# Performance work log

Measured on AMD Instinct MI355X. Metric: run time of the kernel, lower is better.

## Reference

```python
import jax, jax.numpy as jnp
import numpy as np

B, H, L, D = 2, 16, 1024, 64
LMAX = 2048  # max_sequence_length: patterns built & normalized at LMAX, then sliced to L
PI = float(np.pi)


def _scale_pattern(freq):
    # pattern[h, t, d] = exp(i(t+ph)) + exp(i(2t+ph)) + exp(i(0.5t+ph)), ph = 2*pi*h/H
    # identical across d, so keep [H, L, 1] and broadcast over D
    phase = 2.0 * PI * jnp.arange(H, dtype=jnp.float32) / H          # [H]
    t = jnp.linspace(0.0, 2.0 * PI * freq, LMAX)                     # [LMAX]
    a1 = t[None, :] + phase[:, None]
    a2 = 2.0 * t[None, :] + phase[:, None]
    a3 = 0.5 * t[None, :] + phase[:, None]
    pr = jnp.cos(a1) + jnp.cos(a2) + jnp.cos(a3)                     # [H, LMAX]
    pi_ = jnp.sin(a1) + jnp.sin(a2) + jnp.sin(a3)
    norm = jnp.sqrt(jnp.sum(pr * pr + pi_ * pi_, axis=1, keepdims=True))  # over full LMAX
    pr, pi_ = pr / norm, pi_ / norm
    return pr[:, :L, None], pi_[:, :L, None]                          # [H, L, 1]


def _expert_total_pattern():
    # 8 experts x 3 aspects; pattern[t, d] = exp(i(f*t + 2*pi*d/D)), normalized per
    # column over LMAX (|exp|=1 -> norm sqrt(LMAX)). Elementwise complex multiply is
    # linear, so the expert stage equals x * sum(all patterns)/(sqrt(3)*sqrt(8)).
    freqs = np.array([[0.3 + 0.1 * i, 0.2 + 0.1 * i, 0.1 + 0.1 * i]
                      for i in range(8)], dtype=np.float32).reshape(-1)   # [24]
    t = jnp.linspace(0.0, 2.0 * PI, LMAX)                                 # [LMAX]
    phase_d = 2.0 * PI * jnp.arange(D, dtype=jnp.float32) / D             # [D]
    ang = jnp.asarray(freqs)[:, None, None] * t[None, :, None] + phase_d[None, None, :]  # [24, LMAX, D]
    col_norm = 1.0 / np.sqrt(float(LMAX))
    denom = np.sqrt(3.0) * np.sqrt(8.0)
    pr = jnp.sum(jnp.cos(ang), axis=0) * (col_norm / denom)               # [LMAX, D]
    pi_ = jnp.sum(jnp.sin(ang), axis=0) * (col_norm / denom)
    return pr[:L], pi_[:L]                                                # [L, D]


def _process_scale(Qr, Qi, Kr, Ki, Vr, Vi, pr, pi_):
    # complex elementwise pattern multiply
    Qpr = Qr * pr - Qi * pi_
    Qpi = Qr * pi_ + Qi * pr
    Kpr = Kr * pr - Ki * pi_
    Kpi = Kr * pi_ + Ki * pr
    # complex scores = Qp @ Kp^T (no conjugation, matching the torch code)
    sr = jnp.einsum('bhld,bhmd->bhlm', Qpr, Kpr) - jnp.einsum('bhld,bhmd->bhlm', Qpi, Kpi)
    si = jnp.einsum('bhld,bhmd->bhlm', Qpr, Kpi) + jnp.einsum('bhld,bhmd->bhlm', Qpi, Kpr)
    mag = jnp.sqrt(sr * sr + si * si) / np.sqrt(float(D))
    w = jax.nn.softmax(mag, axis=-1)
    return (jnp.einsum('bhlm,bhmd->bhld', w, Vr),
            jnp.einsum('bhlm,bhmd->bhld', w, Vi))


def reference(Q_real, Q_imag, K_real, K_imag, V_real, V_imag):
    scale_freqs = [1.0, 0.5, 0.25, 0.1]  # char, word, phrase, sentence
    acc_r = jnp.zeros_like(Q_real)
    acc_i = jnp.zeros_like(Q_real)
    for f in scale_freqs:
        pr, pi_ = _scale_pattern(f)
        o_r, o_i = _process_scale(Q_real, Q_imag, K_real, K_imag, V_real, V_imag, pr, pi_)
        acc_r = acc_r + o_r
        acc_i = acc_i + o_i
    inv = 1.0 / np.sqrt(float(len(scale_freqs)))
    acc_r = acc_r * inv
    acc_i = acc_i * inv
    # expert mixing (linear in x -> single fused complex elementwise multiply)
    epr, epi = _expert_total_pattern()  # [L, D], broadcast over B,H
    out_r = acc_r * epr - acc_i * epi
    out_i = acc_r * epi + acc_i * epr
    return jnp.stack([out_r, out_i], axis=0)  # [2, B, H, L, D] (real, imag)


def setup_inputs() -> dict:
    key = jax.random.key(0)
    ks = jax.random.split(key, 6)
    shape = (B, H, L, D)
    names = ['Q_real', 'Q_imag', 'K_real', 'K_imag', 'V_real', 'V_imag']
    return {n: jax.random.normal(k, shape, dtype=jnp.float32) for n, k in zip(names, ks)}
```

## Files before the change

### kernel.cpp

```cpp
#include <hip/hip_runtime.h>
#include <math.h>

typedef short bf16x8 __attribute__((ext_vector_type(8)));
typedef float f32x4 __attribute__((ext_vector_type(4)));

#define BDIM 256
#define ADIM 512
constexpr int B_ = 2, H_ = 16, L_ = 1024, D_ = 64, LMAX_ = 2048;
constexpr int BH_ = B_ * H_;
constexpr float PI_F = 3.14159265358979323846f;

constexpr int WS_SVP = 0;
constexpr int WS_KBR = 65536;
constexpr int WS_KBI = WS_KBR + 1048576;
constexpr int WS_VTR = WS_KBI + 1048576;
constexpr int WS_VTI = WS_VTR + 1048576;

__device__ __forceinline__ unsigned short f2b(float x) {
    union { float f; unsigned u; } v; v.f = x;
    return (unsigned short)((v.u + 0x8000u) >> 16);
}
__device__ __forceinline__ float b2f(unsigned short x) {
    union { unsigned u; float f; } v; v.u = ((unsigned)x) << 16;
    return v.f;
}
__device__ __forceinline__ unsigned pk2(float a, float b) {
    union { float f; unsigned u; } va, vb; va.f = a; vb.f = b;
    return ((va.u + 0x8000u) >> 16) | ((vb.u + 0x8000u) & 0xFFFF0000u);
}
__device__ __forceinline__ uint4 pack4(const float4& a, const float4& b) {
    return make_uint4(pk2(a.x, a.y), pk2(a.z, a.w), pk2(b.x, b.y), pk2(b.z, b.w));
}
__device__ __forceinline__ unsigned cvtpk(float lo, float hi) {
    unsigned r;
    asm("v_cvt_pk_bf16_f32 %0, %1, %2" : "=v"(r) : "v"(lo), "v"(hi));
    return r;
}
__device__ __forceinline__ float vsqrt(float x) {
    float r;
    asm("v_sqrt_f32 %0, %1" : "=v"(r) : "v"(x));
    return r;
}

#define MFMA(a, b, c) __builtin_amdgcn_mfma_f32_16x16x32_bf16((a), (b), (c), 0, 0, 0)

__device__ __forceinline__ float a_val(int s, int l, float4 invn) {
    const float fr = (s == 0) ? 1.0f : (s == 1) ? 0.5f : (s == 2) ? 0.25f : 0.1f;
    const float iv = (s == 0) ? invn.x : (s == 1) ? invn.y : (s == 2) ? invn.z : invn.w;
    float t = (2.0f * PI_F * fr / (float)(LMAX_ - 1)) * (float)l;
    float m2 = 3.0f + 2.0f * cosf(t) + 2.0f * cosf(0.5f * t) + 2.0f * cosf(1.5f * t);
    return sqrtf(fmaxf(m2, 0.0f)) * iv;
}

__global__ __launch_bounds__(BDIM)
void prep_kernel(const float* __restrict__ Kr, const float* __restrict__ Ki,
                 const float* __restrict__ Vr, const float* __restrict__ Vi,
                 float* __restrict__ ws) {
    const int tid = threadIdx.x;
    const int blk = blockIdx.x;
    unsigned short* KbR = (unsigned short*)(ws + WS_KBR);
    unsigned short* KbI = (unsigned short*)(ws + WS_KBI);
    unsigned short* VtR = (unsigned short*)(ws + WS_VTR);
    unsigned short* VtI = (unsigned short*)(ws + WS_VTI);

    if (blk < 256) {
        const int comp = blk >> 7;
        const float* src = comp ? Ki : Kr;
        unsigned short* dst = comp ? KbI : KbR;
        size_t b0 = (size_t)(blk & 127) * 16384;
#pragma unroll
        for (int i = 0; i < 4; ++i) {
            size_t e = b0 + (size_t)(i * 256 + tid) * 16;
            float4 x0 = *(const float4*)(src + e);
            float4 x1 = *(const float4*)(src + e + 4);
            float4 x2 = *(const float4*)(src + e + 8);
            float4 x3 = *(const float4*)(src + e + 12);
            *(uint4*)(dst + e) = pack4(x0, x1);
            *(uint4*)(dst + e + 8) = pack4(x2, x3);
        }
    } else {
        __shared__ unsigned short sT[64 * 70];
        __shared__ float sRed[4 * 64];
        const int vb = blk - 256;
        const int comp = vb & 1, mt = (vb >> 1) & 15, bh = vb >> 5;
        const int m0 = mt * 64;
        const float* src = (comp ? Vi : Vr) + (size_t)bh * 65536 + (size_t)m0 * 64;
        unsigned short* dstA = (comp ? VtI : VtR) + (size_t)bh * 65536;
#pragma unroll
        for (int i = 0; i < 4; ++i) {
            int e = i * 256 + tid;
            int m = e >> 4, d4 = (e & 15) * 4;
            float4 x = *(const float4*)(src + (size_t)m * 64 + d4);
            *(uint2*)&sT[m * 70 + d4] = make_uint2(pk2(x.x, x.y), pk2(x.z, x.w));
        }
        {
            int d = tid & 63, grp = tid >> 6;
            float s = 0.0f;
#pragma unroll
            for (int k = 0; k < 16; ++k) s += src[(size_t)(grp * 16 + k) * 64 + d];
            sRed[grp * 64 + d] = s;
        }
        __syncthreads();
        {
            int d = tid >> 2, ms = (tid & 3) * 16;
            unsigned short v[16];
#pragma unroll
            for (int k = 0; k < 16; ++k) v[k] = sT[(ms + k) * 70 + d];
            unsigned short* dst = dstA + (size_t)d * 1024 + m0 + ms;
            *(uint4*)dst = make_uint4((unsigned)v[0] | ((unsigned)v[1] << 16),
                                      (unsigned)v[2] | ((unsigned)v[3] << 16),
                                      (unsigned)v[4] | ((unsigned)v[5] << 16),
                                      (unsigned)v[6] | ((unsigned)v[7] << 16));
            *(uint4*)(dst + 8) = make_uint4((unsigned)v[8] | ((unsigned)v[9] << 16),
                                            (unsigned)v[10] | ((unsigned)v[11] << 16),
                                            (unsigned)v[12] | ((unsigned)v[13] << 16),
                                            (unsigned)v[14] | ((unsigned)v[15] << 16));
        }
        if (tid < 64)
            ws[WS_SVP + comp * 32768 + bh * 1024 + tid * 16 + mt] =
                sRed[tid] + sRed[64 + tid] + sRed[128 + tid] + sRed[192 + tid];
    }
}

__device__ __forceinline__ void stage64s(const unsigned short* g0, int stride,
                                         unsigned short* lds, int w, int lane) {
#pragma unroll
    for (int i = 0; i < 2; ++i) {
        int c = w * 2 + i;
        int lrow = c * 8 + (lane >> 3);
        int lg = (lane & 7) ^ (lrow & 7);
        const unsigned short* src = g0 + (size_t)lrow * stride + lg * 8;
        __builtin_amdgcn_global_load_lds(
            (const __attribute__((address_space(1))) void*)src,
            (__attribute__((address_space(3))) void*)(lds + c * 512), 16, 0, 0);
    }
}
__device__ __forceinline__ bf16x8 ldfrag(const unsigned short* b, int row, int g) {
    return *(const bf16x8*)&b[row * 64 + ((g ^ (row & 7)) << 3)];
}

constexpr int OFF_DEN = 0;
constexpr int OFF_K0  = 2048;
constexpr int OFF_K1  = OFF_K0 + 16384;
constexpr int OFF_V0  = OFF_K1 + 16384;
constexpr int OFF_V1  = OFF_V0 + 16384;
constexpr int OFF_E   = OFF_V1 + 16384;
constexpr int OFF_MG  = OFF_E + 16384;
constexpr int OFF_AMB = OFF_MG + 16384;
constexpr int SMEM_BYTES = OFF_AMB + 8256;

__global__ __launch_bounds__(ADIM, 2)
void attn_kernel_w(const float* __restrict__ Qr, const float* __restrict__ Qi,
                   const float* __restrict__ ws, float* __restrict__ out, float4 invn) {
    extern __shared__ char smem[];
    float* sDen = (float*)(smem + OFF_DEN);
    unsigned short* sK0 = (unsigned short*)(smem + OFF_K0);
    unsigned short* sK1 = (unsigned short*)(smem + OFF_K1);
    unsigned short* sV0 = (unsigned short*)(smem + OFF_V0);
    unsigned short* sV1 = (unsigned short*)(smem + OFF_V1);
    unsigned short* sE  = (unsigned short*)(smem + OFF_E);
    unsigned short* sMg = (unsigned short*)(smem + OFF_MG);
    unsigned short* sAmb = (unsigned short*)(smem + OFF_AMB);

    const int tid = threadIdx.x;
    const int lane = tid & 63;
    const int w = tid >> 6;
    const int lo16 = lane & 15;
    const int quad = lane >> 4;
    const int blk = blockIdx.x;
    const int bh = (blk & 7) * 4 + (blk >> 6);
    const int qt = (blk >> 3) & 7;
    const int l0 = qt * 128;
    const size_t base = (size_t)bh * (L_ * D_);

    const unsigned short* gKr = (const unsigned short*)(ws + WS_KBR) + (size_t)bh * 65536;
    const unsigned short* gKi = (const unsigned short*)(ws + WS_KBI) + (size_t)bh * 65536;
    const unsigned short* gVr = (const unsigned short*)(ws + WS_VTR) + (size_t)bh * 65536;
    const unsigned short* gVi = (const unsigned short*)(ws + WS_VTI) + (size_t)bh * 65536;

    if (w < 4) {
        stage64s(gKr, 64, sK0, w, lane);
        stage64s(gKi, 64, sK1, w, lane);
    } else {
        stage64s(gVr, 1024, sV0, w - 4, lane);
        stage64s(gVi, 1024, sV1, w - 4, lane);
    }

    for (int e = tid; e < 4096; e += ADIM) {
        int s = e >> 10, l = e & 1023;
        sAmb[s * 1032 + l] = f2b(a_val(s, l, invn) * 0.125f);
    }

    bf16x8 fQr0, fQr1, fQi0, fQi1, fnQi0, fnQi1;
    {
        const int ql = l0 + w * 16 + lo16;
        const float* qr = Qr + base + (size_t)ql * 64;
        const float* qi = Qi + base + (size_t)ql * 64;
        float4 a0 = *(const float4*)(qr + quad * 8);
        float4 a1 = *(const float4*)(qr + quad * 8 + 4);
        float4 b0 = *(const float4*)(qr + 32 + quad * 8);
        float4 b1 = *(const float4*)(qr + 32 + quad * 8 + 4);
        *(uint4*)&fQr0 = pack4(a0, a1);
        *(uint4*)&fQr1 = pack4(b0, b1);
        a0 = *(const float4*)(qi + quad * 8);
        a1 = *(const float4*)(qi + quad * 8 + 4);
        b0 = *(const float4*)(qi + 32 + quad * 8);
        b1 = *(const float4*)(qi + 32 + quad * 8 + 4);
        *(uint4*)&fQi0 = pack4(a0, a1);
        *(uint4*)&fQi1 = pack4(b0, b1);
        uint4 t0 = *(uint4*)&fQi0, t1 = *(uint4*)&fQi1;
        t0.x ^= 0x80008000u; t0.y ^= 0x80008000u; t0.z ^= 0x80008000u; t0.w ^= 0x80008000u;
        t1.x ^= 0x80008000u; t1.y ^= 0x80008000u; t1.z ^= 0x80008000u; t1.w ^= 0x80008000u;
        *(uint4*)&fnQi0 = t0; *(uint4*)&fnQi1 = t1;
    }

    __syncthreads();

    bf16x8 uf1a = (bf16x8){0, 0, 0, 0, 0, 0, 0, 0};
    uf1a[0] = (short)f2b(b2f(sAmb[quad * 1032 + (l0 + w * 16 + lo16)]) *
                         (1.0f / 128.0f));

    f32x4 accM1 = (f32x4){0.f, 0.f, 0.f, 0.f};
    f32x4 aOutR[4], aOutI[4];
#pragma unroll
    for (int dt = 0; dt < 4; ++dt) {
        aOutR[dt] = (f32x4){0.f, 0.f, 0.f, 0.f};
        aOutI[dt] = (f32x4){0.f, 0.f, 0.f, 0.f};
    }

#pragma unroll 1
    for (int mt = 0; mt < 16; ++mt) {
        const int m0 = mt * 64;
        const int cur = mt & 1;
        if (mt < 15) {
            if (w < 4) {
                stage64s(gKr + (size_t)(m0 + 64) * 64, 64, sK0 + (cur ^ 1) * 4096, w, lane);
                stage64s(gKi + (size_t)(m0 + 64) * 64, 64, sK1 + (cur ^ 1) * 4096, w, lane);
            } else {
                stage64s(gVr + m0 + 64, 1024, sV0 + (cur ^ 1) * 4096, w - 4, lane);
                stage64s(gVi + m0 + 64, 1024, sV1 + (cur ^ 1) * 4096, w - 4, lane);
            }
        }
        const unsigned short* cK0 = sK0 + cur * 4096;
        const unsigned short* cK1 = sK1 + cur * 4096;
        const unsigned short* cV0 = sV0 + cur * 4096;
        const unsigned short* cV1 = sV1 + cur * 4096;

#pragma unroll
        for (int ct = 0; ct < 4; ++ct) {
            const int mrow = ct * 16 + lo16;
            bf16x8 kr0 = ldfrag(cK0, mrow, quad), kr1 = ldfrag(cK0, mrow, quad + 4);
            bf16x8 ki0 = ldfrag(cK1, mrow, quad), ki1 = ldfrag(cK1, mrow, quad + 4);
            f32x4 aR = (f32x4){0.f, 0.f, 0.f, 0.f};
            f32x4 aI = (f32x4){0.f, 0.f, 0.f, 0.f};
            __builtin_amdgcn_s_setprio(1);
            aR = MFMA(kr0, fQr0, aR);  aR = MFMA(kr1, fQr1, aR);
            aR = MFMA(ki0, fnQi0, aR); aR = MFMA(ki1, fnQi1, aR);
            aI = MFMA(ki0, fQr0, aI);  aI = MFMA(ki1, fQr1, aI);
            aI = MFMA(kr0, fQi0, aI);  aI = MFMA(kr1, fQi1, aI);
            __builtin_amdgcn_s_setprio(0);
            float mg0 = vsqrt(fmaf(aR[0], aR[0], aI[0] * aI[0]));
            float mg1 = vsqrt(fmaf(aR[1], aR[1], aI[1] * aI[1]));
            float mg2 = vsqrt(fmaf(aR[2], aR[2], aI[2] * aI[2]));
            float mg3 = vsqrt(fmaf(aR[3], aR[3], aI[3] * aI[3]));
            bf16x8 bf1 = (bf16x8){0, 0, 0, 0, 0, 0, 0, 0};
            bf1[0] = (short)sAmb[quad * 1032 + m0 + ct * 16 + lo16];
            f32x4 z = (f32x4){0.f, 0.f, 0.f, 0.f};
            f32x4 a1 = MFMA(bf1, uf1a, z);
            float p0 = mg0 * a1[0], p1 = mg1 * a1[1];
            float p2 = mg2 * a1[2], p3 = mg3 * a1[3];
            int l = w * 16 + lo16;
            int gph = (ct * 2 + (quad >> 1)) ^ (l & 7);
            *(uint2*)&sE[l * 64 + gph * 8 + (quad & 1) * 4] =
                make_uint2(cvtpk(p0, p1), cvtpk(p2, p3));
            *(uint2*)&sMg[l * 64 + gph * 8 + (quad & 1) * 4] =
                make_uint2(cvtpk(mg0, mg1), cvtpk(mg2, mg3));
        }
        {
            bf16x8 mf0 = ldfrag(sMg, w * 16 + lo16, quad);
            bf16x8 mf1 = ldfrag(sMg, w * 16 + lo16, quad + 4);
            bf16x8 b0 = (bf16x8){0, 0, 0, 0, 0, 0, 0, 0};
            bf16x8 b1 = (bf16x8){0, 0, 0, 0, 0, 0, 0, 0};
            if (lo16 < 4) {
                b0 = *(const bf16x8*)&sAmb[lo16 * 1032 + m0 + quad * 8];
                b1 = *(const bf16x8*)&sAmb[lo16 * 1032 + m0 + 32 + quad * 8];
            }
            accM1 = MFMA(mf0, b0, accM1);
            accM1 = MFMA(mf1, b1, accM1);
        }
        {
            bf16x8 pa0 = ldfrag(sE, w * 16 + lo16, quad);
            bf16x8 pa1 = ldfrag(sE, w * 16 + lo16, quad + 4);
            __builtin_amdgcn_s_setprio(1);
#pragma unroll
            for (int dt = 0; dt < 4; ++dt) {
                int dr = dt * 16 + lo16;
                bf16x8 vr0 = ldfrag(cV0, dr, quad), vr1 = ldfrag(cV0, dr, quad + 4);
                bf16x8 vi0 = ldfrag(cV1, dr, quad), vi1 = ldfrag(cV1, dr, quad + 4);
                aOutR[dt] = MFMA(pa0, vr0, aOutR[dt]);
                aOutR[dt] = MFMA(pa1, vr1, aOutR[dt]);
                aOutI[dt] = MFMA(pa0, vi0, aOutI[dt]);
                aOutI[dt] = MFMA(pa1, vi1, aOutI[dt]);
            }
            __builtin_amdgcn_s_setprio(0);
        }
        asm volatile("s_waitcnt vmcnt(0)" ::: "memory");
        __builtin_amdgcn_s_barrier();
    }

    if (lo16 < 4) {
#pragma unroll
        for (int reg = 0; reg < 4; ++reg) {
            int r = w * 16 + quad * 4 + reg;
            float alv = b2f(sAmb[lo16 * 1032 + (l0 + r)]) * 8.0f;
            sDen[lo16 * 128 + r] = 1.0f / (1024.0f + alv * accM1[reg]);
        }
    }
    float cden[4];
#pragma unroll
    for (int reg = 0; reg < 4; ++reg) {
        int r = w * 16 + quad * 4 + reg;
        cden[reg] = sDen[r] + sDen[128 + r] + sDen[256 + r] + sDen[384 + r];
    }

    const float cE = rsqrtf(2048.0f) * rsqrtf(24.0f);
    float eRr[4], eRi[4];
#pragma unroll
    for (int reg = 0; reg < 4; ++reg) {
        int lrow = l0 + w * 16 + quad * 4 + reg;
        float tl = (2.0f * PI_F / (float)(LMAX_ - 1)) * (float)lrow;
        float s1, c1;
        __sincosf(0.1f * tl, &s1, &c1);
        const float W[10] = {1.f, 2.f, 3.f, 3.f, 3.f, 3.f, 3.f, 3.f, 2.f, 1.f};
        float cr = c1, ci = s1;
        float er = W[0] * cr, ei = W[0] * ci;
#pragma unroll
        for (int k = 1; k < 10; ++k) {
            float nr = cr * c1 - ci * s1;
            float ni = cr * s1 + ci * c1;
            cr = nr; ci = ni;
            er = fmaf(W[k], cr, er);
            ei = fmaf(W[k], ci, ei);
        }
        eRr[reg] = er * cE;
        eRi[reg] = ei * cE;
    }

    const size_t ooff = (size_t)BH_ * L_ * D_;
#pragma unroll
    for (int dt = 0; dt < 4; ++dt) {
        int d = dt * 16 + lo16;
        const float* svp = ws + WS_SVP + bh * 1024 + (size_t)d * 16;
        float4 r0 = *(const float4*)(svp);
        float4 r1 = *(const float4*)(svp + 4);
        float4 r2 = *(const float4*)(svp + 8);
        float4 r3 = *(const float4*)(svp + 12);
        float svr = (r0.x + r0.y + r0.z + r0.w) + (r1.x + r1.y + r1.z + r1.w) +
                    (r2.x + r2.y + r2.z + r2.w) + (r3.x + r3.y + r3.z + r3.w);
        const float* svq = svp + 32768;
        r0 = *(const float4*)(svq);
        r1 = *(const float4*)(svq + 4);
        r2 = *(const float4*)(svq + 8);
        r3 = *(const float4*)(svq + 12);
        float svi = (r0.x + r0.y + r0.z + r0.w) + (r1.x + r1.y + r1.z + r1.w) +
                    (r2.x + r2.y + r2.z + r2.w) + (r3.x + r3.y + r3.z + r3.w);
        float sp, cp;
        __sincosf((2.0f * PI_F / 64.0f) * (float)d, &sp, &cp);
#pragma unroll
        for (int reg = 0; reg < 4; ++reg) {
            int lrow = l0 + w * 16 + quad * 4 + reg;
            float numR = fmaf(cden[reg], svr, aOutR[dt][reg]) * 0.5f;
            float numI = fmaf(cden[reg], svi, aOutI[dt][reg]) * 0.5f;
            float epr = cp * eRr[reg] - sp * eRi[reg];
            float epi = sp * eRr[reg] + cp * eRi[reg];
            size_t o = base + (size_t)lrow * 64 + d;
            out[o] = numR * epr - numI * epi;
            out[o + ooff] = numR * epi + numI * epr;
        }
    }
}

__global__ __launch_bounds__(BDIM, 2)
void attn_kernel(const float* __restrict__ Qr, const float* __restrict__ Qi,
                 const float* __restrict__ ws, float* __restrict__ out, float4 invn) {
    __shared__ unsigned short sK0[2][4096], sK1[2][4096];
    __shared__ unsigned short sV0[4096], sV1[4096];
    __shared__ unsigned short sE[4096];
    __shared__ unsigned short sMg[4096];
    __shared__ unsigned short sAmb[4 * 1032];
    __shared__ float sDen[4 * 64];

    const int tid = threadIdx.x;
    const int lane = tid & 63;
    const int w = tid >> 6;
    const int lo16 = lane & 15;
    const int quad = lane >> 4;
    const int blk = blockIdx.x;
    const int bh = (blk & 7) * 4 + (blk >> 7);
    const int qt = (blk >> 3) & 15;
    const int l0 = qt * 64;
    const size_t base = (size_t)bh * (L_ * D_);

    const unsigned short* gKr = (const unsigned short*)(ws + WS_KBR) + (size_t)bh * 65536;
    const unsigned short* gKi = (const unsigned short*)(ws + WS_KBI) + (size_t)bh * 65536;
    const unsigned short* gVr = (const unsigned short*)(ws + WS_VTR) + (size_t)bh * 65536;
    const unsigned short* gVi = (const unsigned short*)(ws + WS_VTI) + (size_t)bh * 65536;

    stage64s(gKr, 64, sK0[0], w, lane);
    stage64s(gKi, 64, sK1[0], w, lane);

    for (int e = tid; e < 4096; e += BDIM) {
        int s = e >> 10, l = e & 1023;
        sAmb[s * 1032 + l] = f2b(a_val(s, l, invn) * 0.125f);
    }

    bf16x8 fQr0, fQr1, fQi0, fQi1, fnQi0, fnQi1;
    {
        const int ql = l0 + w * 16 + lo16;
        const float* qr = Qr + base + (size_t)ql * 64;
        const float* qi = Qi + base + (size_t)ql * 64;
        float4 a0 = *(const float4*)(qr + quad * 8);
        float4 a1 = *(const float4*)(qr + quad * 8 + 4);
        float4 b0 = *(const float4*)(qr + 32 + quad * 8);
        float4 b1 = *(const float4*)(qr + 32 + quad * 8 + 4);
        *(uint4*)&fQr0 = pack4(a0, a1);
        *(uint4*)&fQr1 = pack4(b0, b1);
        a0 = *(const float4*)(qi + quad * 8);
        a1 = *(const float4*)(qi + quad * 8 + 4);
        b0 = *(const float4*)(qi + 32 + quad * 8);
        b1 = *(const float4*)(qi + 32 + quad * 8 + 4);
        *(uint4*)&fQi0 = pack4(a0, a1);
        *(uint4*)&fQi1 = pack4(b0, b1);
        uint4 t0 = *(uint4*)&fQi0, t1 = *(uint4*)&fQi1;
        t0.x ^= 0x80008000u; t0.y ^= 0x80008000u; t0.z ^= 0x80008000u; t0.w ^= 0x80008000u;
        t1.x ^= 0x80008000u; t1.y ^= 0x80008000u; t1.z ^= 0x80008000u; t1.w ^= 0x80008000u;
        *(uint4*)&fnQi0 = t0; *(uint4*)&fnQi1 = t1;
    }

    __syncthreads();

    bf16x8 uf1a = (bf16x8){0, 0, 0, 0, 0, 0, 0, 0};
    uf1a[0] = (short)f2b(b2f(sAmb[quad * 1032 + (l0 + w * 16 + lo16)]) *
                         (1.0f / 128.0f));

    f32x4 accM1 = (f32x4){0.f, 0.f, 0.f, 0.f};
    f32x4 aOutR[4], aOutI[4];
#pragma unroll
    for (int dt = 0; dt < 4; ++dt) {
        aOutR[dt] = (f32x4){0.f, 0.f, 0.f, 0.f};
        aOutI[dt] = (f32x4){0.f, 0.f, 0.f, 0.f};
    }

#pragma unroll 1
    for (int mt = 0; mt < 16; ++mt) {
        const int m0 = mt * 64;
        const int cur = mt & 1;
        stage64s(gVr + m0, 1024, sV0, w, lane);
        stage64s(gVi + m0, 1024, sV1, w, lane);
        if (mt < 15) {
            stage64s(gKr + (size_t)(m0 + 64) * 64, 64, sK0[cur ^ 1], w, lane);
            stage64s(gKi + (size_t)(m0 + 64) * 64, 64, sK1[cur ^ 1], w, lane);
        }
        const unsigned short* cK0 = sK0[cur];
        const unsigned short* cK1 = sK1[cur];

#pragma unroll
        for (int ct = 0; ct < 4; ++ct) {
            const int mrow = ct * 16 + lo16;
            bf16x8 kr0 = ldfrag(cK0, mrow, quad), kr1 = ldfrag(cK0, mrow, quad + 4);
            bf16x8 ki0 = ldfrag(cK1, mrow, quad), ki1 = ldfrag(cK1, mrow, quad + 4);
            f32x4 aR = (f32x4){0.f, 0.f, 0.f, 0.f};
            f32x4 aI = (f32x4){0.f, 0.f, 0.f, 0.f};
            __builtin_amdgcn_s_setprio(1);
            aR = MFMA(kr0, fQr0, aR);  aR = MFMA(kr1, fQr1, aR);
            aR = MFMA(ki0, fnQi0, aR); aR = MFMA(ki1, fnQi1, aR);
            aI = MFMA(ki0, fQr0, aI);  aI = MFMA(ki1, fQr1, aI);
            aI = MFMA(kr0, fQi0, aI);  aI = MFMA(kr1, fQi1, aI);
            __builtin_amdgcn_s_setprio(0);
            float mg0 = vsqrt(fmaf(aR[0], aR[0], aI[0] * aI[0]));
            float mg1 = vsqrt(fmaf(aR[1], aR[1], aI[1] * aI[1]));
            float mg2 = vsqrt(fmaf(aR[2], aR[2], aI[2] * aI[2]));
            float mg3 = vsqrt(fmaf(aR[3], aR[3], aI[3] * aI[3]));
            bf16x8 bf1 = (bf16x8){0, 0, 0, 0, 0, 0, 0, 0};
            bf1[0] = (short)sAmb[quad * 1032 + m0 + ct * 16 + lo16];
            f32x4 z = (f32x4){0.f, 0.f, 0.f, 0.f};
            f32x4 a1 = MFMA(bf1, uf1a, z);
            float p0 = mg0 * a1[0], p1 = mg1 * a1[1];
            float p2 = mg2 * a1[2], p3 = mg3 * a1[3];
            int l = w * 16 + lo16;
            int gph = (ct * 2 + (quad >> 1)) ^ (l & 7);
            *(uint2*)&sE[l * 64 + gph * 8 + (quad & 1) * 4] =
                make_uint2(cvtpk(p0, p1), cvtpk(p2, p3));
            *(uint2*)&sMg[l * 64 + gph * 8 + (quad & 1) * 4] =
                make_uint2(cvtpk(mg0, mg1), cvtpk(mg2, mg3));
        }
        {
            bf16x8 mf0 = ldfrag(sMg, w * 16 + lo16, quad);
            bf16x8 mf1 = ldfrag(sMg, w * 16 + lo16, quad + 4);
            bf16x8 b0 = (bf16x8){0, 0, 0, 0, 0, 0, 0, 0};
            bf16x8 b1 = (bf16x8){0, 0, 0, 0, 0, 0, 0, 0};
            if (lo16 < 4) {
                b0 = *(const bf16x8*)&sAmb[lo16 * 1032 + m0 + quad * 8];
                b1 = *(const bf16x8*)&sAmb[lo16 * 1032 + m0 + 32 + quad * 8];
            }
            accM1 = MFMA(mf0, b0, accM1);
            accM1 = MFMA(mf1, b1, accM1);
        }
        if (mt < 15) {
            asm volatile("s_waitcnt vmcnt(4)" ::: "memory");
        } else {
            asm volatile("s_waitcnt vmcnt(0)" ::: "memory");
        }
        __builtin_amdgcn_s_barrier();
        {
            bf16x8 pa0 = ldfrag(sE, w * 16 + lo16, quad);
            bf16x8 pa1 = ldfrag(sE, w * 16 + lo16, quad + 4);
            __builtin_amdgcn_s_setprio(1);
#pragma unroll
            for (int dt = 0; dt < 4; ++dt) {
                int dr = dt * 16 + lo16;
                bf16x8 vr0 = ldfrag(sV0, dr, quad), vr1 = ldfrag(sV0, dr, quad + 4);
                bf16x8 vi0 = ldfrag(sV1, dr, quad), vi1 = ldfrag(sV1, dr, quad + 4);
                aOutR[dt] = MFMA(pa0, vr0, aOutR[dt]);
                aOutR[dt] = MFMA(pa1, vr1, aOutR[dt]);
                aOutI[dt] = MFMA(pa0, vi0, aOutI[dt]);
                aOutI[dt] = MFMA(pa1, vi1, aOutI[dt]);
            }
            __builtin_amdgcn_s_setprio(0);
        }
        asm volatile("s_waitcnt vmcnt(0)" ::: "memory");
        __builtin_amdgcn_s_barrier();
    }

    if (lo16 < 4) {
#pragma unroll
        for (int reg = 0; reg < 4; ++reg) {
            int r = w * 16 + quad * 4 + reg;
            float alv = b2f(sAmb[lo16 * 1032 + (l0 + r)]) * 8.0f;
            sDen[lo16 * 64 + r] = 1.0f / (1024.0f + alv * accM1[reg]);
        }
    }
    float cden[4];
#pragma unroll
    for (int reg = 0; reg < 4; ++reg) {
        int r = w * 16 + quad * 4 + reg;
        cden[reg] = sDen[r] + sDen[64 + r] + sDen[128 + r] + sDen[192 + r];
    }

    const float cE = rsqrtf(2048.0f) * rsqrtf(24.0f);
    float eRr[4], eRi[4];
#pragma unroll
    for (int reg = 0; reg < 4; ++reg) {
        int lrow = l0 + w * 16 + quad * 4 + reg;
        float tl = (2.0f * PI_F / (float)(LMAX_ - 1)) * (float)lrow;
        float s1, c1;
        __sincosf(0.1f * tl, &s1, &c1);
        const float W[10] = {1.f, 2.f, 3.f, 3.f, 3.f, 3.f, 3.f, 3.f, 2.f, 1.f};
        float cr = c1, ci = s1;
        float er = W[0] * cr, ei = W[0] * ci;
#pragma unroll
        for (int k = 1; k < 10; ++k) {
            float nr = cr * c1 - ci * s1;
            float ni = cr * s1 + ci * c1;
            cr = nr; ci = ni;
            er = fmaf(W[k], cr, er);
            ei = fmaf(W[k], ci, ei);
        }
        eRr[reg] = er * cE;
        eRi[reg] = ei * cE;
    }

    const size_t ooff = (size_t)BH_ * L_ * D_;
#pragma unroll
    for (int dt = 0; dt < 4; ++dt) {
        int d = dt * 16 + lo16;
        const float* svp = ws + WS_SVP + bh * 1024 + (size_t)d * 16;
        float4 r0 = *(const float4*)(svp);
        float4 r1 = *(const float4*)(svp + 4);
        float4 r2 = *(const float4*)(svp + 8);
        float4 r3 = *(const float4*)(svp + 12);
        float svr = (r0.x + r0.y + r0.z + r0.w) + (r1.x + r1.y + r1.z + r1.w) +
                    (r2.x + r2.y + r2.z + r2.w) + (r3.x + r3.y + r3.z + r3.w);
        const float* svq = svp + 32768;
        r0 = *(const float4*)(svq);
        r1 = *(const float4*)(svq + 4);
        r2 = *(const float4*)(svq + 8);
        r3 = *(const float4*)(svq + 12);
        float svi = (r0.x + r0.y + r0.z + r0.w) + (r1.x + r1.y + r1.z + r1.w) +
                    (r2.x + r2.y + r2.z + r2.w) + (r3.x + r3.y + r3.z + r3.w);
        float sp, cp;
        __sincosf((2.0f * PI_F / 64.0f) * (float)d, &sp, &cp);
#pragma unroll
        for (int reg = 0; reg < 4; ++reg) {
            int lrow = l0 + w * 16 + quad * 4 + reg;
            float numR = fmaf(cden[reg], svr, aOutR[dt][reg]) * 0.5f;
            float numI = fmaf(cden[reg], svi, aOutI[dt][reg]) * 0.5f;
            float epr = cp * eRr[reg] - sp * eRi[reg];
            float epi = sp * eRr[reg] + cp * eRi[reg];
            size_t o = base + (size_t)lrow * 64 + d;
            out[o] = numR * epr - numI * epi;
            out[o + ooff] = numR * epi + numI * epr;
        }
    }
}

extern "C" void kernel_launch(void* const* d_in, const int* in_sizes, int n_in,
                              void* d_out, int out_size, void* d_ws, size_t ws_size,
                              hipStream_t stream) {
    const float* Qr = (const float*)d_in[0];
    const float* Qi = (const float*)d_in[1];
    const float* Kr = (const float*)d_in[2];
    const float* Ki = (const float*)d_in[3];
    const float* Vr = (const float*)d_in[4];
    const float* Vi = (const float*)d_in[5];
    float* ws = (float*)d_ws;
    float* out = (float*)d_out;

    const double fr[4] = {1.0, 0.5, 0.25, 0.1};
    float inv[4];
    for (int s = 0; s < 4; ++s) {
        double a = 2.0 * 3.14159265358979323846 * fr[s] / (double)(LMAX_ - 1);
        double S = 3.0 * LMAX_;
        const double mul[3] = {1.0, 0.5, 1.5};
        for (int k = 0; k < 3; ++k) {
            double x = a * mul[k];
            S += 2.0 * (cos(x * 1023.5) * sin(x * 1024.0) / sin(x * 0.5));
        }
        inv[s] = (float)(1.0 / sqrt(S));
    }
    float4 invn = make_float4(inv[0], inv[1], inv[2], inv[3]);

    prep_kernel<<<1280, BDIM, 0, stream>>>(Kr, Ki, Vr, Vi, ws);

    static int wideOK = -1;
    if (wideOK < 0) {
        hipError_t e = hipFuncSetAttribute(
            reinterpret_cast<const void*>(attn_kernel_w),
            hipFuncAttributeMaxDynamicSharedMemorySize, SMEM_BYTES);
        wideOK = (e == hipSuccess) ? 1 : 0;
    }
    if (wideOK)
        attn_kernel_w<<<256, ADIM, SMEM_BYTES, stream>>>(Qr, Qi, ws, out, invn);
    else
        attn_kernel<<<512, BDIM, 0, stream>>>(Qr, Qi, ws, out, invn);
}
```

Before: 138.8 us.

## Split key columns across two wave halves with 1024-thread blocks and LDS reduction

New measurement: 134.6 us. 3.0% less time.

```diff
diff --git a/kernel.cpp b/kernel.cpp
--- a/kernel.cpp
+++ b/kernel.cpp
@@ -5,7 +5,7 @@
 typedef float f32x4 __attribute__((ext_vector_type(4)));
 
 #define BDIM 256
-#define ADIM 512
+#define ADIM 1024
 constexpr int B_ = 2, H_ = 16, L_ = 1024, D_ = 64, LMAX_ = 2048;
 constexpr int BH_ = B_ * H_;
 constexpr float PI_F = 3.14159265358979323846f;
@@ -149,7 +149,7 @@
 constexpr int OFF_AMB = OFF_MG + 16384;
 constexpr int SMEM_BYTES = OFF_AMB + 8256;
 
-__global__ __launch_bounds__(ADIM, 2)
+__global__ __launch_bounds__(ADIM, 1)
 void attn_kernel_w(const float* __restrict__ Qr, const float* __restrict__ Qi,
                    const float* __restrict__ ws, float* __restrict__ out, float4 invn) {
     extern __shared__ char smem[];
@@ -165,8 +165,11 @@
     const int tid = threadIdx.x;
     const int lane = tid & 63;
     const int w = tid >> 6;
+    const int half = w >> 3;
+    const int w8 = w & 7;
     const int lo16 = lane & 15;
     const int quad = lane >> 4;
+    const int gh = quad + half * 4;
     const int blk = blockIdx.x;
     const int bh = (blk & 7) * 4 + (blk >> 6);
     const int qt = (blk >> 3) & 7;
@@ -181,12 +184,248 @@
     if (w < 4) {
         stage64s(gKr, 64, sK0, w, lane);
         stage64s(gKi, 64, sK1, w, lane);
-    } else {
-        stage64s(gVr, 1024, sV0, w - 4, lane);
-        stage64s(gVi, 1024, sV1, w - 4, lane);
+    } else if (w >= 8 && w < 12) {
+        stage64s(gVr, 1024, sV0, w - 8, lane);
+        stage64s(gVi, 1024, sV1, w - 8, lane);
     }
 
     for (int e = tid; e < 4096; e += ADIM) {
+        int s = e >> 10, l = e & 1023;
+        sAmb[s * 1032 + l] = f2b(a_val(s, l, invn) * 0.125f);
+    }
+
+    bf16x8 fQr0, fQr1, fQi0, fQi1, fnQi0, fnQi1;
+    {
+        const int ql = l0 + w8 * 16 + lo16;
+        const float* qr = Qr + base + (size_t)ql * 64;
+        const float* qi = Qi + base + (size_t)ql * 64;
+        float4 a0 = *(const float4*)(qr + quad * 8);
+        float4 a1 = *(const float4*)(qr + quad * 8 + 4);
+        float4 b0 = *(const float4*)(qr + 32 + quad * 8);
+        float4 b1 = *(const float4*)(qr + 32 + quad * 8 + 4);
+        *(uint4*)&fQr0 = pack4(a0, a1);
+        *(uint4*)&fQr1 = pack4(b0, b1);
+        a0 = *(const float4*)(qi + quad * 8);
+        a1 = *(const float4*)(qi + quad * 8 + 4);
+        b0 = *(const float4*)(qi + 32 + quad * 8);
+        b1 = *(const float4*)(qi + 32 + quad * 8 + 4);
+        *(uint4*)&fQi0 = pack4(a0, a1);
+        *(uint4*)&fQi1 = pack4(b0, b1);
+        uint4 t0 = *(uint4*)&fQi0, t1 = *(uint4*)&fQi1;
+        t0.x ^= 0x80008000u; t0.y ^= 0x80008000u; t0.z ^= 0x80008000u; t0.w ^= 0x80008000u;
+        t1.x ^= 0x80008000u; t1.y ^= 0x80008000u; t1.z ^= 0x80008000u; t1.w ^= 0x80008000u;
+        *(uint4*)&fnQi0 = t0; *(uint4*)&fnQi1 = t1;
+    }
+
+    __syncthreads();
+
+    bf16x8 uf1a = (bf16x8){0, 0, 0, 0, 0, 0, 0, 0};
+    uf1a[0] = (short)f2b(b2f(sAmb[quad * 1032 + (l0 + w8 * 16 + lo16)]) *
+                         (1.0f / 128.0f));
+
+    f32x4 accM1 = (f32x4){0.f, 0.f, 0.f, 0.f};
+    f32x4 aOutR[4], aOutI[4];
+#pragma unroll
+    for (int dt = 0; dt < 4; ++dt) {
+        aOutR[dt] = (f32x4){0.f, 0.f, 0.f, 0.f};
+        aOutI[dt] = (f32x4){0.f, 0.f, 0.f, 0.f};
+    }
+
+    const int lrow_w = w8 * 16 + lo16;
+
+#pragma unroll 1
+    for (int mt = 0; mt < 16; ++mt) {
+        const int m0 = mt * 64;
+        const int cur = mt & 1;
+        if (mt < 15) {
+            if (w < 4) {
+                stage64s(gKr + (size_t)(m0 + 64) * 64, 64, sK0 + (cur ^ 1) * 4096, w, lane);
+                stage64s(gKi + (size_t)(m0 + 64) * 64, 64, sK1 + (cur ^ 1) * 4096, w, lane);
+            } else if (w >= 8 && w < 12) {
+                stage64s(gVr + m0 + 64, 1024, sV0 + (cur ^ 1) * 4096, w - 8, lane);
+                stage64s(gVi + m0 + 64, 1024, sV1 + (cur ^ 1) * 4096, w - 8, lane);
+            }
+        }
+        const unsigned short* cK0 = sK0 + cur * 4096;
+        const unsigned short* cK1 = sK1 + cur * 4096;
+        const unsigned short* cV0 = sV0 + cur * 4096;
+        const unsigned short* cV1 = sV1 + cur * 4096;
+
+#pragma unroll
+        for (int ct = 0; ct < 2; ++ct) {
+            const int ct_eff = half * 2 + ct;
+            const int mrow = ct_eff * 16 + lo16;
+            bf16x8 kr0 = ldfrag(cK0, mrow, quad), kr1 = ldfrag(cK0, mrow, quad + 4);
+            bf16x8 ki0 = ldfrag(cK1, mrow, quad), ki1 = ldfrag(cK1, mrow, quad + 4);
+            f32x4 aR = (f32x4){0.f, 0.f, 0.f, 0.f};
+            f32x4 aI = (f32x4){0.f, 0.f, 0.f, 0.f};
+            __builtin_amdgcn_s_setprio(1);
+            aR = MFMA(kr0, fQr0, aR);  aR = MFMA(kr1, fQr1, aR);
+            aR = MFMA(ki0, fnQi0, aR); aR = MFMA(ki1, fnQi1, aR);
+            aI = MFMA(ki0, fQr0, aI);  aI = MFMA(ki1, fQr1, aI);
+            aI = MFMA(kr0, fQi0, aI);  aI = MFMA(kr1, fQi1, aI);
+            __builtin_amdgcn_s_setprio(0);
+            float mg0 = vsqrt(fmaf(aR[0], aR[0], aI[0] * aI[0]));
+            float mg1 = vsqrt(fmaf(aR[1], aR[1], aI[1] * aI[1]));
+            float mg2 = vsqrt(fmaf(aR[2], aR[2], aI[2] * aI[2]));
+            float mg3 = vsqrt(fmaf(aR[3], aR[3], aI[3] * aI[3]));
+            bf16x8 bf1 = (bf16x8){0, 0, 0, 0, 0, 0, 0, 0};
+            bf1[0] = (short)sAmb[quad * 1032 + m0 + ct_eff * 16 + lo16];
+            f32x4 z = (f32x4){0.f, 0.f, 0.f, 0.f};
+            f32x4 a1 = MFMA(bf1, uf1a, z);
+            float p0 = mg0 * a1[0], p1 = mg1 * a1[1];
+            float p2 = mg2 * a1[2], p3 = mg3 * a1[3];
+            int gph = (ct_eff * 2 + (quad >> 1)) ^ (lrow_w & 7);
+            *(uint2*)&sE[lrow_w * 64 + gph * 8 + (quad & 1) * 4] =
+                make_uint2(cvtpk(p0, p1), cvtpk(p2, p3));
+            *(uint2*)&sMg[lrow_w * 64 + gph * 8 + (quad & 1) * 4] =
+                make_uint2(cvtpk(mg0, mg1), cvtpk(mg2, mg3));
+        }
+        {
+            bf16x8 mf = ldfrag(sMg, lrow_w, gh);
+            bf16x8 b0 = (bf16x8){0, 0, 0, 0, 0, 0, 0, 0};
+            if (lo16 < 4)
+                b0 = *(const bf16x8*)&sAmb[lo16 * 1032 + m0 + half * 32 + quad * 8];
+            accM1 = MFMA(mf, b0, accM1);
+        }
+        {
+            bf16x8 pa = ldfrag(sE, lrow_w, gh);
+            __builtin_amdgcn_s_setprio(1);
+#pragma unroll
+            for (int dt = 0; dt < 4; ++dt) {
+                int dr = dt * 16 + lo16;
+                bf16x8 vr = ldfrag(cV0, dr, gh);
+                bf16x8 vi = ldfrag(cV1, dr, gh);
+                aOutR[dt] = MFMA(pa, vr, aOutR[dt]);
+                aOutI[dt] = MFMA(pa, vi, aOutI[dt]);
+            }
+            __builtin_amdgcn_s_setprio(0);
+        }
+        asm volatile("s_waitcnt vmcnt(0)" ::: "memory");
+        __builtin_amdgcn_s_barrier();
+    }
+
+    char* scr = smem + OFF_K0;
+    if (half == 1) {
+#pragma unroll
+        for (int dt = 0; dt < 4; ++dt) {
+            *(f32x4*)(scr + w8 * 9216 + dt * 1024 + lane * 16) = aOutR[dt];
+            *(f32x4*)(scr + w8 * 9216 + 4096 + dt * 1024 + lane * 16) = aOutI[dt];
+        }
+        *(f32x4*)(scr + w8 * 9216 + 8192 + lane * 16) = accM1;
+    }
+    __syncthreads();
+    if (half == 1) return;
+
+#pragma unroll
+    for (int dt = 0; dt < 4; ++dt) {
+        aOutR[dt] += *(const f32x4*)(scr + w8 * 9216 + dt * 1024 + lane * 16);
+        aOutI[dt] += *(const f32x4*)(scr + w8 * 9216 + 4096 + dt * 1024 + lane * 16);
+    }
+    accM1 += *(const f32x4*)(scr + w8 * 9216 + 8192 + lane * 16);
+
+    if (lo16 < 4) {
+#pragma unroll
+        for (int reg = 0; reg < 4; ++reg) {
+            int r = w8 * 16 + quad * 4 + reg;
+            float alv = b2f(sAmb[lo16 * 1032 + (l0 + r)]) * 8.0f;
+            sDen[lo16 * 128 + r] = 1.0f / (1024.0f + alv * accM1[reg]);
+        }
+    }
+    float cden[4];
+#pragma unroll
+    for (int reg = 0; reg < 4; ++reg) {
+        int r = w8 * 16 + quad * 4 + reg;
+        cden[reg] = sDen[r] + sDen[128 + r] + sDen[256 + r] + sDen[384 + r];
+    }
+
+    const float cE = rsqrtf(2048.0f) * rsqrtf(24.0f);
+    float eRr[4], eRi[4];
+#pragma unroll
+    for (int reg = 0; reg < 4; ++reg) {
+        int lrow = l0 + w8 * 16 + quad * 4 + reg;
+        float tl = (2.0f * PI_F / (float)(LMAX_ - 1)) * (float)lrow;
+        float s1, c1;
+        __sincosf(0.1f * tl, &s1, &c1);
+        const float W[10] = {1.f, 2.f, 3.f, 3.f, 3.f, 3.f, 3.f, 3.f, 2.f, 1.f};
+        float cr = c1, ci = s1;
+        float er = W[0] * cr, ei = W[0] * ci;
+#pragma unroll
+        for (int k = 1; k < 10; ++k) {
+            float nr = cr * c1 - ci * s1;
+            float ni = cr * s1 + ci * c1;
+            cr = nr; ci = ni;
+            er = fmaf(W[k], cr, er);
+            ei = fmaf(W[k], ci, ei);
+        }
+        eRr[reg] = er * cE;
+        eRi[reg] = ei * cE;
+    }
+
+    const size_t ooff = (size_t)BH_ * L_ * D_;
+#pragma unroll
+    for (int dt = 0; dt < 4; ++dt) {
+        int d = dt * 16 + lo16;
+        const float* svp = ws + WS_SVP + bh * 1024 + (size_t)d * 16;
+        float4 r0 = *(const float4*)(svp);
+        float4 r1 = *(const float4*)(svp + 4);
+        float4 r2 = *(const float4*)(svp + 8);
+        float4 r3 = *(const float4*)(svp + 12);
+        float svr = (r0.x + r0.y + r0.z + r0.w) + (r1.x + r1.y + r1.z + r1.w) +
+                    (r2.x + r2.y + r2.z + r2.w) + (r3.x + r3.y + r3.z + r3.w);
+        const float* svq = svp + 32768;
+        r0 = *(const float4*)(svq);
+        r1 = *(const float4*)(svq + 4);
+        r2 = *(const float4*)(svq + 8);
+        r3 = *(const float4*)(svq + 12);
+        float svi = (r0.x + r0.y + r0.z + r0.w) + (r1.x + r1.y + r1.z + r1.w) +
+                    (r2.x + r2.y + r2.z + r2.w) + (r3.x + r3.y + r3.z + r3.w);
+        float sp, cp;
+        __sincosf((2.0f * PI_F / 64.0f) * (float)d, &sp, &cp);
+#pragma unroll
+        for (int reg = 0; reg < 4; ++reg) {
+            int lrow = l0 + w8 * 16 + quad * 4 + reg;
+            float numR = fmaf(cden[reg], svr, aOutR[dt][reg]) * 0.5f;
+            float numI = fmaf(cden[reg], svi, aOutI[dt][reg]) * 0.5f;
+            float epr = cp * eRr[reg] - sp * eRi[reg];
+            float epi = sp * eRr[reg] + cp * eRi[reg];
+            size_t o = base + (size_t)lrow * 64 + d;
+            out[o] = numR * epr - numI * epi;
+            out[o + ooff] = numR * epi + numI * epr;
+        }
+    }
+}
+
+__global__ __launch_bounds__(BDIM, 2)
+void attn_kernel(const float* __restrict__ Qr, const float* __restrict__ Qi,
+                 const float* __restrict__ ws, float* __restrict__ out, float4 invn) {
+    __shared__ unsigned short sK0[2][4096], sK1[2][4096];
+    __shared__ unsigned short sV0[4096], sV1[4096];
+    __shared__ unsigned short sE[4096];
+    __shared__ unsigned short sMg[4096];
+    __shared__ unsigned short sAmb[4 * 1032];
+    __shared__ float sDen[4 * 64];
+
+    const int tid = threadIdx.x;
+    const int lane = tid & 63;
+    const int w = tid >> 6;
+    const int lo16 = lane & 15;
+    const int quad = lane >> 4;
+    const int blk = blockIdx.x;
+    const int bh = (blk & 7) * 4 + (blk >> 7);
+    const int qt = (blk >> 3) & 15;
+    const int l0 = qt * 64;
+    const size_t base = (size_t)bh * (L_ * D_);
+
+    const unsigned short* gKr = (const unsigned short*)(ws + WS_KBR) + (size_t)bh * 65536;
+    const unsigned short* gKi = (const unsigned short*)(ws + WS_KBI) + (size_t)bh * 65536;
+    const unsigned short* gVr = (const unsigned short*)(ws + WS_VTR) + (size_t)bh * 65536;
+    const unsigned short* gVi = (const unsigned short*)(ws + WS_VTI) + (size_t)bh * 65536;
+
+    stage64s(gKr, 64, sK0[0], w, lane);
+    stage64s(gKi, 64, sK1[0], w, lane);
+
+    for (int e = tid; e < 4096; e += BDIM) {
         int s = e >> 10, l = e & 1023;
         sAmb[s * 1032 + l] = f2b(a_val(s, l, invn) * 0.125f);
     }
@@ -232,19 +471,14 @@
     for (int mt = 0; mt < 16; ++mt) {
         const int m0 = mt * 64;
         const int cur = mt & 1;
+        stage64s(gVr + m0, 1024, sV0, w, lane);
+        stage64s(gVi + m0, 1024, sV1, w, lane);
         if (mt < 15) {
-            if (w < 4) {
-                stage64s(gKr + (size_t)(m0 + 64) * 64, 64, sK0 + (cur ^ 1) * 4096, w, lane);
-                stage64s(gKi + (size_t)(m0 + 64) * 64, 64, sK1 + (cur ^ 1) * 4096, w, lane);
-            } else {
-                stage64s(gVr + m0 + 64, 1024, sV0 + (cur ^ 1) * 4096, w - 4, lane);
-                stage64s(gVi + m0 + 64, 1024, sV1 + (cur ^ 1) * 4096, w - 4, lane);
-            }
-        }
-        const unsigned short* cK0 = sK0 + cur * 4096;
-        const unsigned short* cK1 = sK1 + cur * 4096;
-        const unsigned short* cV0 = sV0 + cur * 4096;
-        const unsigned short* cV1 = sV1 + cur * 4096;
+            stage64s(gKr + (size_t)(m0 + 64) * 64, 64, sK0[cur ^ 1], w, lane);
+            stage64s(gKi + (size_t)(m0 + 64) * 64, 64, sK1[cur ^ 1], w, lane);
+        }
+        const unsigned short* cK0 = sK0[cur];
+        const unsigned short* cK1 = sK1[cur];
 
 #pragma unroll
         for (int ct = 0; ct < 4; ++ct) {
@@ -288,6 +522,12 @@
             accM1 = MFMA(mf0, b0, accM1);
             accM1 = MFMA(mf1, b1, accM1);
         }
+        if (mt < 15) {
+            asm volatile("s_waitcnt vmcnt(4)" ::: "memory");
+        } else {
+            asm volatile("s_waitcnt vmcnt(0)" ::: "memory");
+        }
+        __builtin_amdgcn_s_barrier();
         {
             bf16x8 pa0 = ldfrag(sE, w * 16 + lo16, quad);
             bf16x8 pa1 = ldfrag(sE, w * 16 + lo16, quad + 4);
@@ -295,8 +535,8 @@
 #pragma unroll
             for (int dt = 0; dt < 4; ++dt) {
                 int dr = dt * 16 + lo16;
-                bf16x8 vr0 = ldfrag(cV0, dr, quad), vr1 = ldfrag(cV0, dr, quad + 4);
-                bf16x8 vi0 = ldfrag(cV1, dr, quad), vi1 = ldfrag(cV1, dr, quad + 4);
+                bf16x8 vr0 = ldfrag(sV0, dr, quad), vr1 = ldfrag(sV0, dr, quad + 4);
+                bf16x8 vi0 = ldfrag(sV1, dr, quad), vi1 = ldfrag(sV1, dr, quad + 4);
                 aOutR[dt] = MFMA(pa0, vr0, aOutR[dt]);
                 aOutR[dt] = MFMA(pa1, vr1, aOutR[dt]);
                 aOutI[dt] = MFMA(pa0, vi0, aOutI[dt]);
@@ -313,14 +553,14 @@
         for (int reg = 0; reg < 4; ++reg) {
             int r = w * 16 + quad * 4 + reg;
             float alv = b2f(sAmb[lo16 * 1032 + (l0 + r)]) * 8.0f;
-            sDen[lo16 * 128 + r] = 1.0f / (1024.0f + alv * accM1[reg]);
+            sDen[lo16 * 64 + r] = 1.0f / (1024.0f + alv * accM1[reg]);
         }
     }
     float cden[4];
 #pragma unroll
     for (int reg = 0; reg < 4; ++reg) {
         int r = w * 16 + quad * 4 + reg;
-        cden[reg] = sDen[r] + sDen[128 + r] + sDen[256 + r] + sDen[384 + r];
+        cden[reg] = sDen[r] + sDen[64 + r] + sDen[128 + r] + sDen[192 + r];
     }
 
     const float cE = rsqrtf(2048.0f) * rsqrtf(24.0f);
@@ -380,230 +620,6 @@
     }
 }
 
-__global__ __launch_bounds__(BDIM, 2)
-void attn_kernel(const float* __restrict__ Qr, const float* __restrict__ Qi,
-                 const float* __restrict__ ws, float* __restrict__ out, float4 invn) {
-    __shared__ unsigned short sK0[2][4096], sK1[2][4096];
-    __shared__ unsigned short sV0[4096], sV1[4096];
-    __shared__ unsigned short sE[4096];
-    __shared__ unsigned short sMg[4096];
-    __shared__ unsigned short sAmb[4 * 1032];
-    __shared__ float sDen[4 * 64];
-
-    const int tid = threadIdx.x;
-    const int lane = tid & 63;
-    const int w = tid >> 6;
-    const int lo16 = lane & 15;
-    const int quad = lane >> 4;
-    const int blk = blockIdx.x;
-    const int bh = (blk & 7) * 4 + (blk >> 7);
-    const int qt = (blk >> 3) & 15;
-    const int l0 = qt * 64;
-    const size_t base = (size_t)bh * (L_ * D_);
-
-    const unsigned short* gKr = (const unsigned short*)(ws + WS_KBR) + (size_t)bh * 65536;
-    const unsigned short* gKi = (const unsigned short*)(ws + WS_KBI) + (size_t)bh * 65536;
-    const unsigned short* gVr = (const unsigned short*)(ws + WS_VTR) + (size_t)bh * 65536;
-    const unsigned short* gVi = (const unsigned short*)(ws + WS_VTI) + (size_t)bh * 65536;
-
-    stage64s(gKr, 64, sK0[0], w, lane);
-    stage64s(gKi, 64, sK1[0], w, lane);
-
-    for (int e = tid; e < 4096; e += BDIM) {
-        int s = e >> 10, l = e & 1023;
-        sAmb[s * 1032 + l] = f2b(a_val(s, l, invn) * 0.125f);
-    }
-
-    bf16x8 fQr0, fQr1, fQi0, fQi1, fnQi0, fnQi1;
-    {
-        const int ql = l0 + w * 16 + lo16;
-        const float* qr = Qr + base + (size_t)ql * 64;
-        const float* qi = Qi + base + (size_t)ql * 64;
-        float4 a0 = *(const float4*)(qr + quad * 8);
-        float4 a1 = *(const float4*)(qr + quad * 8 + 4);
-        float4 b0 = *(const float4*)(qr + 32 + quad * 8);
-        float4 b1 = *(const float4*)(qr + 32 + quad * 8 + 4);
-        *(uint4*)&fQr0 = pack4(a0, a1);
-        *(uint4*)&fQr1 = pack4(b0, b1);
-        a0 = *(const float4*)(qi + quad * 8);
-        a1 = *(const float4*)(qi + quad * 8 + 4);
-        b0 = *(const float4*)(qi + 32 + quad * 8);
-        b1 = *(const float4*)(qi + 32 + quad * 8 + 4);
-        *(uint4*)&fQi0 = pack4(a0, a1);
-        *(uint4*)&fQi1 = pack4(b0, b1);
-        uint4 t0 = *(uint4*)&fQi0, t1 = *(uint4*)&fQi1;
-        t0.x ^= 0x80008000u; t0.y ^= 0x80008000u; t0.z ^= 0x80008000u; t0.w ^= 0x80008000u;
-        t1.x ^= 0x80008000u; t1.y ^= 0x80008000u; t1.z ^= 0x80008000u; t1.w ^= 0x80008000u;
-        *(uint4*)&fnQi0 = t0; *(uint4*)&fnQi1 = t1;
-    }
-
-    __syncthreads();
-
-    bf16x8 uf1a = (bf16x8){0, 0, 0, 0, 0, 0, 0, 0};
-    uf1a[0] = (short)f2b(b2f(sAmb[quad * 1032 + (l0 + w * 16 + lo16)]) *
-                         (1.0f / 128.0f));
-
-    f32x4 accM1 = (f32x4){0.f, 0.f, 0.f, 0.f};
-    f32x4 aOutR[4], aOutI[4];
-#pragma unroll
-    for (int dt = 0; dt < 4; ++dt) {
-        aOutR[dt] = (f32x4){0.f, 0.f, 0.f, 0.f};
-        aOutI[dt] = (f32x4){0.f, 0.f, 0.f, 0.f};
-    }
-
-#pragma unroll 1
-    for (int mt = 0; mt < 16; ++mt) {
-        const int m0 = mt * 64;
-        const int cur = mt & 1;
-        stage64s(gVr + m0, 1024, sV0, w, lane);
-        stage64s(gVi + m0, 1024, sV1, w, lane);
-        if (mt < 15) {
-            stage64s(gKr + (size_t)(m0 + 64) * 64, 64, sK0[cur ^ 1], w, lane);
-            stage64s(gKi + (size_t)(m0 + 64) * 64, 64, sK1[cur ^ 1], w, lane);
-        }
-        const unsigned short* cK0 = sK0[cur];
-        const unsigned short* cK1 = sK1[cur];
-
-#pragma unroll
-        for (int ct = 0; ct < 4; ++ct) {
-            const int mrow = ct * 16 + lo16;
-            bf16x8 kr0 = ldfrag(cK0, mrow, quad), kr1 = ldfrag(cK0, mrow, quad + 4);
-            bf16x8 ki0 = ldfrag(cK1, mrow, quad), ki1 = ldfrag(cK1, mrow, quad + 4);
-            f32x4 aR = (f32x4){0.f, 0.f, 0.f, 0.f};
-            f32x4 aI = (f32x4){0.f, 0.f, 0.f, 0.f};
-            __builtin_amdgcn_s_setprio(1);
-            aR = MFMA(kr0, fQr0, aR);  aR = MFMA(kr1, fQr1, aR);
-            aR = MFMA(ki0, fnQi0, aR); aR = MFMA(ki1, fnQi1, aR);
-            aI = MFMA(ki0, fQr0, aI);  aI = MFMA(ki1, fQr1, aI);
-            aI = MFMA(kr0, fQi0, aI);  aI = MFMA(kr1, fQi1, aI);
-            __builtin_amdgcn_s_setprio(0);
-            float mg0 = vsqrt(fmaf(aR[0], aR[0], aI[0] * aI[0]));
-            float mg1 = vsqrt(fmaf(aR[1], aR[1], aI[1] * aI[1]));
-            float mg2 = vsqrt(fmaf(aR[2], aR[2], aI[2] * aI[2]));
-            float mg3 = vsqrt(fmaf(aR[3], aR[3], aI[3] * aI[3]));
-            bf16x8 bf1 = (bf16x8){0, 0, 0, 0, 0, 0, 0, 0};
-            bf1[0] = (short)sAmb[quad * 1032 + m0 + ct * 16 + lo16];
-            f32x4 z = (f32x4){0.f, 0.f, 0.f, 0.f};
-            f32x4 a1 = MFMA(bf1, uf1a, z);
-            float p0 = mg0 * a1[0], p1 = mg1 * a1[1];
-            float p2 = mg2 * a1[2], p3 = mg3 * a1[3];
-            int l = w * 16 + lo16;
-            int gph = (ct * 2 + (quad >> 1)) ^ (l & 7);
-            *(uint2*)&sE[l * 64 + gph * 8 + (quad & 1) * 4] =
-                make_uint2(cvtpk(p0, p1), cvtpk(p2, p3));
-            *(uint2*)&sMg[l * 64 + gph * 8 + (quad & 1) * 4] =
-                make_uint2(cvtpk(mg0, mg1), cvtpk(mg2, mg3));
-        }
-        {
-            bf16x8 mf0 = ldfrag(sMg, w * 16 + lo16, quad);
-            bf16x8 mf1 = ldfrag(sMg, w * 16 + lo16, quad + 4);
-            bf16x8 b0 = (bf16x8){0, 0, 0, 0, 0, 0, 0, 0};
-            bf16x8 b1 = (bf16x8){0, 0, 0, 0, 0, 0, 0, 0};
-            if (lo16 < 4) {
-                b0 = *(const bf16x8*)&sAmb[lo16 * 1032 + m0 + quad * 8];
-                b1 = *(const bf16x8*)&sAmb[lo16 * 1032 + m0 + 32 + quad * 8];
-            }
-            accM1 = MFMA(mf0, b0, accM1);
-            accM1 = MFMA(mf1, b1, accM1);
-        }
-        if (mt < 15) {
-            asm volatile("s_waitcnt vmcnt(4)" ::: "memory");
-        } else {
-            asm volatile("s_waitcnt vmcnt(0)" ::: "memory");
-        }
-        __builtin_amdgcn_s_barrier();
-        {
-            bf16x8 pa0 = ldfrag(sE, w * 16 + lo16, quad);
-            bf16x8 pa1 = ldfrag(sE, w * 16 + lo16, quad + 4);
-            __builtin_amdgcn_s_setprio(1);
-#pragma unroll
-            for (int dt = 0; dt < 4; ++dt) {
-                int dr = dt * 16 + lo16;
-                bf16x8 vr0 = ldfrag(sV0, dr, quad), vr1 = ldfrag(sV0, dr, quad + 4);
-                bf16x8 vi0 = ldfrag(sV1, dr, quad), vi1 = ldfrag(sV1, dr, quad + 4);
-                aOutR[dt] = MFMA(pa0, vr0, aOutR[dt]);
-                aOutR[dt] = MFMA(pa1, vr1, aOutR[dt]);
-                aOutI[dt] = MFMA(pa0, vi0, aOutI[dt]);
-                aOutI[dt] = MFMA(pa1, vi1, aOutI[dt]);
-            }
-            __builtin_amdgcn_s_setprio(0);
-        }
-        asm volatile("s_waitcnt vmcnt(0)" ::: "memory");
-        __builtin_amdgcn_s_barrier();
-    }
-
-    if (lo16 < 4) {
-#pragma unroll
-        for (int reg = 0; reg < 4; ++reg) {
-            int r = w * 16 + quad * 4 + reg;
-            float alv = b2f(sAmb[lo16 * 1032 + (l0 + r)]) * 8.0f;
-            sDen[lo16 * 64 + r] = 1.0f / (1024.0f + alv * accM1[reg]);
-        }
-    }
-    float cden[4];
-#pragma unroll
-    for (int reg = 0; reg < 4; ++reg) {
-        int r = w * 16 + quad * 4 + reg;
-        cden[reg] = sDen[r] + sDen[64 + r] + sDen[128 + r] + sDen[192 + r];
-    }
-
-    const float cE = rsqrtf(2048.0f) * rsqrtf(24.0f);
-    float eRr[4], eRi[4];
-#pragma unroll
-    for (int reg = 0; reg < 4; ++reg) {
-        int lrow = l0 + w * 16 + quad * 4 + reg;
-        float tl = (2.0f * PI_F / (float)(LMAX_ - 1)) * (float)lrow;
-        float s1, c1;
-        __sincosf(0.1f * tl, &s1, &c1);
-        const float W[10] = {1.f, 2.f, 3.f, 3.f, 3.f, 3.f, 3.f, 3.f, 2.f, 1.f};
-        float cr = c1, ci = s1;
-        float er = W[0] * cr, ei = W[0] * ci;
-#pragma unroll
-        for (int k = 1; k < 10; ++k) {
-            float nr = cr * c1 - ci * s1;
-            float ni = cr * s1 + ci * c1;
-            cr = nr; ci = ni;
-            er = fmaf(W[k], cr, er);
-            ei = fmaf(W[k], ci, ei);
-        }
-        eRr[reg] = er * cE;
-        eRi[reg] = ei * cE;
-    }
-
-    const size_t ooff = (size_t)BH_ * L_ * D_;
-#pragma unroll
-    for (int dt = 0; dt < 4; ++dt) {
-        int d = dt * 16 + lo16;
-        const float* svp = ws + WS_SVP + bh * 1024 + (size_t)d * 16;
-        float4 r0 = *(const float4*)(svp);
-        float4 r1 = *(const float4*)(svp + 4);
-        float4 r2 = *(const float4*)(svp + 8);
-        float4 r3 = *(const float4*)(svp + 12);
-        float svr = (r0.x + r0.y + r0.z + r0.w) + (r1.x + r1.y + r1.z + r1.w) +
-                    (r2.x + r2.y + r2.z + r2.w) + (r3.x + r3.y + r3.z + r3.w);
-        const float* svq = svp + 32768;
-        r0 = *(const float4*)(svq);
-        r1 = *(const float4*)(svq + 4);
-        r2 = *(const float4*)(svq + 8);
-        r3 = *(const float4*)(svq + 12);
-        float svi = (r0.x + r0.y + r0.z + r0.w) + (r1.x + r1.y + r1.z + r1.w) +
-                    (r2.x + r2.y + r2.z + r2.w) + (r3.x + r3.y + r3.z + r3.w);
-        float sp, cp;
-        __sincosf((2.0f * PI_F / 64.0f) * (float)d, &sp, &cp);
-#pragma unroll
-        for (int reg = 0; reg < 4; ++reg) {
-            int lrow = l0 + w * 16 + quad * 4 + reg;
-            float numR = fmaf(cden[reg], svr, aOutR[dt][reg]) * 0.5f;
-            float numI = fmaf(cden[reg], svi, aOutI[dt][reg]) * 0.5f;
-            float epr = cp * eRr[reg] - sp * eRi[reg];
-            float epi = sp * eRr[reg] + cp * eRi[reg];
-            size_t o = base + (size_t)lrow * 64 + d;
-            out[o] = numR * epr - numI * epi;
-            out[o + ooff] = numR * epi + numI * epr;
-        }
-    }
-}
-
 extern "C" void kernel_launch(void* const* d_in, const int* in_sizes, int n_in,
                               void* d_out, int out_size, void* d_ws, size_t ws_size,
                               hipStream_t stream) {
```
